# Kernel tuning notes

Measured on AMD Instinct MI355X. Metric: run time of the kernel, lower is better.

The kernel has to match this reference:

```python
import jax, jax.numpy as jnp
import numpy as np

EPS = 1e-9
THRESHOLD = 0.2          # second_policy_eval = 'threshold'
CAP_FACTOR = 2.0         # capacity_factor_eval
MIN_EXPERT_CAPACITY = 4


def setup_inputs() -> dict:
    key = jax.random.key(0)
    k1, k2 = jax.random.split(key)
    x = jax.random.normal(k1, (8, 2048, 1024), dtype=jnp.float32)
    W = jax.random.normal(k2, (1024, 64), dtype=jnp.float32) * 0.02
    return {"x": x, "W": W}


def _cumsum_exclusive(t):
    # exclusive cumsum along token dim (-2)
    return jnp.cumsum(t, axis=-2) - t


def reference(x, W):
    b, n, d = x.shape
    e = W.shape[1]
    dt = x.dtype

    raw_gates = jax.nn.softmax(jnp.einsum('bnd,de->bne', x, W), axis=-1)  # [b,n,e]

    gate_1 = jnp.max(raw_gates, axis=-1)            # [b,n]
    index_1 = jnp.argmax(raw_gates, axis=-1)        # [b,n]
    mask_1 = jax.nn.one_hot(index_1, e, dtype=dt)   # [b,n,e]
    density_1_proxy = raw_gates

    gates_wo_top1 = raw_gates * (1.0 - mask_1)
    gate_2 = jnp.max(gates_wo_top1, axis=-1)
    index_2 = jnp.argmax(gates_wo_top1, axis=-1)
    mask_2 = jax.nn.one_hot(index_2, e, dtype=dt)

    denom = gate_1 + gate_2 + EPS
    gate_1 = gate_1 / denom
    gate_2 = gate_2 / denom

    density_1 = jnp.mean(mask_1, axis=-2)                         # [b,e]
    density_1_proxy_m = jnp.mean(density_1_proxy, axis=-2)        # [b,e]
    loss = jnp.mean(density_1_proxy_m * density_1) * float(e ** 2)

    # policy == 'threshold'
    mask_2 = mask_2 * (gate_2 > THRESHOLD).astype(dt)[..., None]

    expert_capacity = max(min(n, int(n * CAP_FACTOR / e)), MIN_EXPERT_CAPACITY)
    cap_f = float(expert_capacity)

    position_in_expert_1 = _cumsum_exclusive(mask_1) * mask_1
    mask_1 = mask_1 * (position_in_expert_1 < cap_f).astype(dt)
    mask_1_count = jnp.sum(mask_1, axis=-2, keepdims=True)        # [b,1,e]
    mask_1_flat = jnp.sum(mask_1, axis=-1)                        # [b,n]
    position_in_expert_1 = jnp.sum(position_in_expert_1, axis=-1) # [b,n]
    gate_1 = gate_1 * mask_1_flat

    position_in_expert_2 = _cumsum_exclusive(mask_2) + mask_1_count
    position_in_expert_2 = position_in_expert_2 * mask_2
    mask_2 = mask_2 * (position_in_expert_2 < cap_f).astype(dt)
    mask_2_flat = jnp.sum(mask_2, axis=-1)
    position_in_expert_2 = jnp.sum(position_in_expert_2, axis=-1)
    gate_2 = gate_2 * mask_2_flat

    # combine: [b, n, e, capacity]
    oh_e1 = jax.nn.one_hot(index_1, e, dtype=dt)[..., None]                                    # [b,n,e,1]
    oh_c1 = jax.nn.one_hot(position_in_expert_1.astype(jnp.int32), expert_capacity, dtype=dt)[..., None, :]  # [b,n,1,cap]
    oh_e2 = jax.nn.one_hot(index_2, e, dtype=dt)[..., None]
    oh_c2 = jax.nn.one_hot(position_in_expert_2.astype(jnp.int32), expert_capacity, dtype=dt)[..., None, :]

    combine_tensor = (
        (gate_1 * mask_1_flat)[..., None, None] * oh_e1 * oh_c1
        + (gate_2 * mask_2_flat)[..., None, None] * oh_e2 * oh_c2
    )
    dispatch_tensor = (combine_tensor != 0).astype(dt)
    return dispatch_tensor, combine_tensor, loss
```

## Files before the change

kernel.cpp:

```cpp
#include <hip/hip_runtime.h>
#include <math.h>

#define BB 8
#define NN 2048
#define DD 1024
#define EE 64
#define CAP 64
#define NTOK (BB * NN)
#define OUT_T_FLOATS 67108864
#define OUT_T_F4     16777216


__global__ __launch_bounds__(1024, 4) void gating_kernel(
    const float* __restrict__ x, const float* __restrict__ W,
    float4* __restrict__ recs, float* __restrict__ dens)
{
    __shared__ float red[4][64][65];
    __shared__ float dred[4][64];

    const int tid  = threadIdx.x;
    const int lane = tid & 63;
    const int wave = __builtin_amdgcn_readfirstlane(tid >> 6);
    const int ks   = wave & 3;
    const int eq   = wave >> 2;
    const int tok  = blockIdx.x * 64 + lane;

    float acc[16];
#pragma unroll
    for (int j = 0; j < 16; ++j) acc[j] = 0.f;

    const float4* xq = (const float4*)(x + (size_t)tok * DD + ks * 256);
    const float*  wq = W + (size_t)(ks * 256) * EE + eq * 16;

#pragma unroll 2
    for (int c = 0; c < 64; ++c) {
        const float4 xv = xq[c];
        const float xs[4] = {xv.x, xv.y, xv.z, xv.w};
#pragma unroll
        for (int kk = 0; kk < 4; ++kk) {
            const float4* wr = (const float4*)(wq + (size_t)(c * 4 + kk) * EE);
            const float4 w0 = wr[0], w1 = wr[1], w2 = wr[2], w3 = wr[3];
            acc[ 0] = fmaf(xs[kk], w0.x, acc[ 0]);
            acc[ 1] = fmaf(xs[kk], w0.y, acc[ 1]);
            acc[ 2] = fmaf(xs[kk], w0.z, acc[ 2]);
            acc[ 3] = fmaf(xs[kk], w0.w, acc[ 3]);
            acc[ 4] = fmaf(xs[kk], w1.x, acc[ 4]);
            acc[ 5] = fmaf(xs[kk], w1.y, acc[ 5]);
            acc[ 6] = fmaf(xs[kk], w1.z, acc[ 6]);
            acc[ 7] = fmaf(xs[kk], w1.w, acc[ 7]);
            acc[ 8] = fmaf(xs[kk], w2.x, acc[ 8]);
            acc[ 9] = fmaf(xs[kk], w2.y, acc[ 9]);
            acc[10] = fmaf(xs[kk], w2.z, acc[10]);
            acc[11] = fmaf(xs[kk], w2.w, acc[11]);
            acc[12] = fmaf(xs[kk], w3.x, acc[12]);
            acc[13] = fmaf(xs[kk], w3.y, acc[13]);
            acc[14] = fmaf(xs[kk], w3.z, acc[14]);
            acc[15] = fmaf(xs[kk], w3.w, acc[15]);
        }
    }

#pragma unroll
    for (int j = 0; j < 16; ++j)
        red[ks][eq * 16 + j][lane] = acc[j];
    __syncthreads();

    if (wave < 4) {
        const int t0 = wave * 16;
        float densacc = 0.f;
#pragma unroll 1
        for (int ti = 0; ti < 16; ++ti) {
            const int t = t0 + ti;
            const float lv = ((red[0][lane][t] + red[1][lane][t])
                            + red[2][lane][t]) + red[3][lane][t];

            float v = lv; int bi = lane;
#pragma unroll
            for (int off = 32; off; off >>= 1) {
                float ov = __shfl_xor(v, off);
                int   oi = __shfl_xor(bi, off);
                if (ov > v || (ov == v && oi < bi)) { v = ov; bi = oi; }
            }
            const float m1 = v; const int i1 = bi;
            float v2 = (lane == i1) ? -INFINITY : lv; int b2 = lane;
#pragma unroll
            for (int off = 32; off; off >>= 1) {
                float ov = __shfl_xor(v2, off);
                int   oi = __shfl_xor(b2, off);
                if (ov > v2 || (ov == v2 && oi < b2)) { v2 = ov; b2 = oi; }
            }
            const float m2 = v2; const int i2 = b2;

            float ex = expf(lv - m1);
            float Z = ex;
#pragma unroll
            for (int off = 32; off; off >>= 1) Z += __shfl_xor(Z, off);
            float g1 = 1.0f / Z;
            float g2 = expf(m2 - m1) * g1;
            float den = g1 + g2 + 1e-9f;
            float g1n = g1 / den;
            float g2n = g2 / den;
            int flag = (g2n > 0.2f) ? 1 : 0;

            densacc += ex * g1;

            if (lane == 0)
                recs[blockIdx.x * 64 + t] =
                    make_float4(g1n, g2n, __int_as_float(i1),
                                __int_as_float(i2 | (flag << 8)));
        }
        dred[wave][lane] = densacc;
    }
    __syncthreads();
    if (tid < 64) {
        float s = dred[0][tid] + dred[1][tid] + dred[2][tid] + dred[3][tid];
        dens[blockIdx.x * 64 + tid] = s;
    }
}

__global__ __launch_bounds__(1024) void scan_kernel(
    const float4* __restrict__ recs, const float* __restrict__ dens,
    float4* __restrict__ frecs, float* __restrict__ lossp)
{
    const int b = blockIdx.x;
    __shared__ int hist1[32][64], pre1[32][64];
    __shared__ int hist2[32][64], pre2[32][64];
    __shared__ int base2[64];
    __shared__ float dsum[64];

    const int tid = threadIdx.x;
    const int lane = tid & 63;
    const int wave = tid >> 6;

    float4 r[2];
    int e1[2], e2[2], fl[2], rank1[2], rank2[2];
    const unsigned long long below = (1ull << lane) - 1ull;

#pragma unroll
    for (int u = 0; u < 2; ++u) {
        const int g = 2 * wave + u;
        const int tok = g * 64 + lane;
        float4 rr = recs[b * NN + tok];
        r[u] = rr;
        e1[u] = __float_as_int(rr.z);
        int i2f = __float_as_int(rr.w);
        e2[u] = i2f & 63;
        fl[u] = i2f >> 8;

        unsigned long long m = ~0ull, mv = ~0ull;
#pragma unroll
        for (int bit = 0; bit < 6; ++bit) {
            unsigned long long vt = __ballot((e1[u] >> bit) & 1);
            m  &= ((e1[u] >> bit) & 1) ? vt : ~vt;
            mv &= ((lane  >> bit) & 1) ? vt : ~vt;
        }
        rank1[u] = __popcll(m & below);
        hist1[g][lane] = __popcll(mv);

        unsigned long long fv = __ballot(fl[u]);
        m = fv; mv = fv;
#pragma unroll
        for (int bit = 0; bit < 6; ++bit) {
            unsigned long long vt = __ballot((e2[u] >> bit) & 1);
            m  &= ((e2[u] >> bit) & 1) ? vt : ~vt;
            mv &= ((lane  >> bit) & 1) ? vt : ~vt;
        }
        rank2[u] = __popcll(m & below);
        hist2[g][lane] = __popcll(mv);
    }

    if (wave == 0) {
        float s = 0.f;
        for (int k = 0; k < 32; ++k) s += dens[(b * 32 + k) * 64 + lane];
        dsum[lane] = s;
    }
    __syncthreads();

    if (wave == 0) {
        int run = 0;
#pragma unroll
        for (int g = 0; g < 32; ++g) { pre1[g][lane] = run; run += hist1[g][lane]; }
        base2[lane] = run < CAP ? run : CAP;
        int run2 = 0;
#pragma unroll
        for (int g = 0; g < 32; ++g) { pre2[g][lane] = run2; run2 += hist2[g][lane]; }
        float v = dsum[lane] * (float)run;
#pragma unroll
        for (int off = 32; off; off >>= 1) v += __shfl_xor(v, off);
        if (lane == 0) lossp[b] = v;
    }
    __syncthreads();

#pragma unroll
    for (int u = 0; u < 2; ++u) {
        const int g = 2 * wave + u;
        const int tok = g * 64 + lane;
        int p1 = rank1[u] + pre1[g][e1[u]];
        int k1 = p1 < CAP;
        int p2 = rank2[u] + pre2[g][e2[u]] + base2[e2[u]];
        int k2 = fl[u] && (p2 < CAP);
        float4 fr;
        fr.x = k1 ? r[u].x : 0.f;
        fr.y = k2 ? r[u].y : 0.f;
        fr.z = __int_as_float(k1 ? (e1[u] * CAP + p1) : -1);
        fr.w = __int_as_float(k2 ? (e2[u] * CAP + p2) : -1);
        frecs[b * NN + tok] = fr;
    }
}

__global__ __launch_bounds__(256) void fill_kernel(
    const float4* __restrict__ frecs, const float* __restrict__ lossp,
    float* __restrict__ out)
{
    const int tid = blockIdx.x * 256 + threadIdx.x;
    const int token = tid >> 10;
    const int e  = (tid >> 4) & 63;
    const int c4 = tid & 15;
    float4 r = frecs[token];

    float cx = 0.f, cy = 0.f, cz = 0.f, cw = 0.f;
    float dx = 0.f, dy = 0.f, dz = 0.f, dw = 0.f;

    int p1 = __float_as_int(r.z);
    if (p1 >= 0 && (p1 >> 6) == e && ((p1 >> 2) & 15) == c4) {
        int cc = p1 & 3;
        if      (cc == 0) { cx = r.x; dx = 1.f; }
        else if (cc == 1) { cy = r.x; dy = 1.f; }
        else if (cc == 2) { cz = r.x; dz = 1.f; }
        else              { cw = r.x; dw = 1.f; }
    }
    int p2 = __float_as_int(r.w);
    if (p2 >= 0 && (p2 >> 6) == e && ((p2 >> 2) & 15) == c4) {
        int cc = p2 & 3;
        if      (cc == 0) { cx = r.y; dx = 1.f; }
        else if (cc == 1) { cy = r.y; dy = 1.f; }
        else if (cc == 2) { cz = r.y; dz = 1.f; }
        else              { cw = r.y; dw = 1.f; }
    }

    float4* o4 = (float4*)out;
    o4[tid]             = make_float4(dx, dy, dz, dw);
    o4[tid + OUT_T_F4]  = make_float4(cx, cy, cz, cw);

    if (tid == 0) {
        float s = 0.f;
        for (int k = 0; k < 8; ++k) s += lossp[k];
        out[2 * (size_t)OUT_T_FLOATS] = s * (1.0f / 524288.0f);
    }
}

extern "C" void kernel_launch(void* const* d_in, const int* in_sizes, int n_in,
                              void* d_out, int out_size, void* d_ws, size_t ws_size,
                              hipStream_t stream)
{
    const float* x = (const float*)d_in[0];
    const float* W = (const float*)d_in[1];
    float* out = (float*)d_out;
    char* ws = (char*)d_ws;

    float4* recs  = (float4*)(ws);
    float4* frecs = (float4*)(ws + 262144);
    float*  dens  = (float*)(ws + 524288);
    float*  lossp = (float*)(ws + 589824);

    gating_kernel<<<256, 1024, 0, stream>>>(x, W, recs, dens);
    scan_kernel<<<8, 1024, 0, stream>>>(recs, dens, frecs, lossp);
    fill_kernel<<<65536, 256, 0, stream>>>(frecs, lossp, out);
}
```

Measured before the change: 609.2 us.

## Stage x tiles in swizzled shared memory and use grid-stride nontemporal fill

```diff
diff --git a/kernel.cpp b/kernel.cpp
--- a/kernel.cpp
+++ b/kernel.cpp
@@ -10,11 +10,14 @@
 #define OUT_T_FLOATS 67108864
 #define OUT_T_F4     16777216
 
+typedef float f32x4 __attribute__((ext_vector_type(4)));
+
 
 __global__ __launch_bounds__(1024, 4) void gating_kernel(
     const float* __restrict__ x, const float* __restrict__ W,
     float4* __restrict__ recs, float* __restrict__ dens)
 {
+    __shared__ float lxs[2][64][128];
     __shared__ float red[4][64][65];
     __shared__ float dred[4][64];
 
@@ -23,40 +26,72 @@
     const int wave = __builtin_amdgcn_readfirstlane(tid >> 6);
     const int ks   = wave & 3;
     const int eq   = wave >> 2;
-    const int tok  = blockIdx.x * 64 + lane;
+    const int tok0 = blockIdx.x * 64;
+
+    const int p  = tid & 31;
+    const int r0 = tid >> 5;
+    const int r1 = r0 + 32;
+    const int g0 = p ^ (r0 & 7);
+    const float* src0 = x + (size_t)(tok0 + r0) * DD + (size_t)g0 * 4;
+    const float* src1 = x + (size_t)(tok0 + r1) * DD + (size_t)g0 * 4;
 
     float acc[16];
 #pragma unroll
     for (int j = 0; j < 16; ++j) acc[j] = 0.f;
 
-    const float4* xq = (const float4*)(x + (size_t)tok * DD + ks * 256);
-    const float*  wq = W + (size_t)(ks * 256) * EE + eq * 16;
-
-#pragma unroll 2
-    for (int c = 0; c < 64; ++c) {
-        const float4 xv = xq[c];
-        const float xs[4] = {xv.x, xv.y, xv.z, xv.w};
-#pragma unroll
-        for (int kk = 0; kk < 4; ++kk) {
-            const float4* wr = (const float4*)(wq + (size_t)(c * 4 + kk) * EE);
-            const float4 w0 = wr[0], w1 = wr[1], w2 = wr[2], w3 = wr[3];
-            acc[ 0] = fmaf(xs[kk], w0.x, acc[ 0]);
-            acc[ 1] = fmaf(xs[kk], w0.y, acc[ 1]);
-            acc[ 2] = fmaf(xs[kk], w0.z, acc[ 2]);
-            acc[ 3] = fmaf(xs[kk], w0.w, acc[ 3]);
-            acc[ 4] = fmaf(xs[kk], w1.x, acc[ 4]);
-            acc[ 5] = fmaf(xs[kk], w1.y, acc[ 5]);
-            acc[ 6] = fmaf(xs[kk], w1.z, acc[ 6]);
-            acc[ 7] = fmaf(xs[kk], w1.w, acc[ 7]);
-            acc[ 8] = fmaf(xs[kk], w2.x, acc[ 8]);
-            acc[ 9] = fmaf(xs[kk], w2.y, acc[ 9]);
-            acc[10] = fmaf(xs[kk], w2.z, acc[10]);
-            acc[11] = fmaf(xs[kk], w2.w, acc[11]);
-            acc[12] = fmaf(xs[kk], w3.x, acc[12]);
-            acc[13] = fmaf(xs[kk], w3.y, acc[13]);
-            acc[14] = fmaf(xs[kk], w3.z, acc[14]);
-            acc[15] = fmaf(xs[kk], w3.w, acc[15]);
-        }
+    {
+        const float4 v0 = *(const float4*)src0;
+        const float4 v1 = *(const float4*)src1;
+        *((float4*)&lxs[0][r0][0] + p) = v0;
+        *((float4*)&lxs[0][r1][0] + p) = v1;
+    }
+    __syncthreads();
+
+    int cur = 0;
+#pragma unroll 1
+    for (int step = 0; step < 8; ++step) {
+        float4 n0, n1;
+        if (step < 7) {
+            n0 = *(const float4*)(src0 + (size_t)(step + 1) * 128);
+            n1 = *(const float4*)(src1 + (size_t)(step + 1) * 128);
+        }
+
+        const float* wbase = W + (size_t)(step * 128 + ks * 32) * EE + eq * 16;
+#pragma unroll
+        for (int kqi = 0; kqi < 8; ++kqi) {
+            const int kq = ks * 8 + kqi;
+            const float4 xv = *((const float4*)&lxs[cur][lane][0] + (kq ^ (lane & 7)));
+            const float xs[4] = {xv.x, xv.y, xv.z, xv.w};
+            const float* wr = wbase + (size_t)(kqi * 4) * EE;
+#pragma unroll
+            for (int kk = 0; kk < 4; ++kk) {
+                const float4* w4 = (const float4*)(wr + (size_t)kk * EE);
+                const float4 w0 = w4[0], w1 = w4[1], w2 = w4[2], w3 = w4[3];
+                acc[ 0] = fmaf(xs[kk], w0.x, acc[ 0]);
+                acc[ 1] = fmaf(xs[kk], w0.y, acc[ 1]);
+                acc[ 2] = fmaf(xs[kk], w0.z, acc[ 2]);
+                acc[ 3] = fmaf(xs[kk], w0.w, acc[ 3]);
+                acc[ 4] = fmaf(xs[kk], w1.x, acc[ 4]);
+                acc[ 5] = fmaf(xs[kk], w1.y, acc[ 5]);
+                acc[ 6] = fmaf(xs[kk], w1.z, acc[ 6]);
+                acc[ 7] = fmaf(xs[kk], w1.w, acc[ 7]);
+                acc[ 8] = fmaf(xs[kk], w2.x, acc[ 8]);
+                acc[ 9] = fmaf(xs[kk], w2.y, acc[ 9]);
+                acc[10] = fmaf(xs[kk], w2.z, acc[10]);
+                acc[11] = fmaf(xs[kk], w2.w, acc[11]);
+                acc[12] = fmaf(xs[kk], w3.x, acc[12]);
+                acc[13] = fmaf(xs[kk], w3.y, acc[13]);
+                acc[14] = fmaf(xs[kk], w3.z, acc[14]);
+                acc[15] = fmaf(xs[kk], w3.w, acc[15]);
+            }
+        }
+
+        if (step < 7) {
+            *((float4*)&lxs[cur ^ 1][r0][0] + p) = n0;
+            *((float4*)&lxs[cur ^ 1][r1][0] + p) = n1;
+        }
+        __syncthreads();
+        cur ^= 1;
     }
 
 #pragma unroll
@@ -211,37 +246,41 @@
     const float4* __restrict__ frecs, const float* __restrict__ lossp,
     float* __restrict__ out)
 {
-    const int tid = blockIdx.x * 256 + threadIdx.x;
-    const int token = tid >> 10;
-    const int e  = (tid >> 4) & 63;
-    const int c4 = tid & 15;
-    float4 r = frecs[token];
-
-    float cx = 0.f, cy = 0.f, cz = 0.f, cw = 0.f;
-    float dx = 0.f, dy = 0.f, dz = 0.f, dw = 0.f;
-
-    int p1 = __float_as_int(r.z);
-    if (p1 >= 0 && (p1 >> 6) == e && ((p1 >> 2) & 15) == c4) {
-        int cc = p1 & 3;
-        if      (cc == 0) { cx = r.x; dx = 1.f; }
-        else if (cc == 1) { cy = r.x; dy = 1.f; }
-        else if (cc == 2) { cz = r.x; dz = 1.f; }
-        else              { cw = r.x; dw = 1.f; }
-    }
-    int p2 = __float_as_int(r.w);
-    if (p2 >= 0 && (p2 >> 6) == e && ((p2 >> 2) & 15) == c4) {
-        int cc = p2 & 3;
-        if      (cc == 0) { cx = r.y; dx = 1.f; }
-        else if (cc == 1) { cy = r.y; dy = 1.f; }
-        else if (cc == 2) { cz = r.y; dz = 1.f; }
-        else              { cw = r.y; dw = 1.f; }
-    }
-
-    float4* o4 = (float4*)out;
-    o4[tid]             = make_float4(dx, dy, dz, dw);
-    o4[tid + OUT_T_F4]  = make_float4(cx, cy, cz, cw);
-
-    if (tid == 0) {
+    f32x4* o4 = (f32x4*)out;
+    const int stride = gridDim.x * 256;
+
+    for (int tid = blockIdx.x * 256 + threadIdx.x; tid < OUT_T_F4; tid += stride) {
+        const int e  = (tid >> 4) & 63;
+        const int c4 = tid & 15;
+        float4 r = frecs[tid >> 10];
+
+        float cx = 0.f, cy = 0.f, cz = 0.f, cw = 0.f;
+        float dx = 0.f, dy = 0.f, dz = 0.f, dw = 0.f;
+
+        int p1 = __float_as_int(r.z);
+        if (p1 >= 0 && (p1 >> 6) == e && ((p1 >> 2) & 15) == c4) {
+            int cc = p1 & 3;
+            if      (cc == 0) { cx = r.x; dx = 1.f; }
+            else if (cc == 1) { cy = r.x; dy = 1.f; }
+            else if (cc == 2) { cz = r.x; dz = 1.f; }
+            else              { cw = r.x; dw = 1.f; }
+        }
+        int p2 = __float_as_int(r.w);
+        if (p2 >= 0 && (p2 >> 6) == e && ((p2 >> 2) & 15) == c4) {
+            int cc = p2 & 3;
+            if      (cc == 0) { cx = r.y; dx = 1.f; }
+            else if (cc == 1) { cy = r.y; dy = 1.f; }
+            else if (cc == 2) { cz = r.y; dz = 1.f; }
+            else              { cw = r.y; dw = 1.f; }
+        }
+
+        f32x4 dv = {dx, dy, dz, dw};
+        f32x4 cv = {cx, cy, cz, cw};
+        __builtin_nontemporal_store(dv, &o4[tid]);
+        __builtin_nontemporal_store(cv, &o4[tid + OUT_T_F4]);
+    }
+
+    if (blockIdx.x == 0 && threadIdx.x == 0) {
         float s = 0.f;
         for (int k = 0; k < 8; ++k) s += lossp[k];
         out[2 * (size_t)OUT_T_FLOATS] = s * (1.0f / 524288.0f);
@@ -264,5 +303,5 @@
 
     gating_kernel<<<256, 1024, 0, stream>>>(x, W, recs, dens);
     scan_kernel<<<8, 1024, 0, stream>>>(recs, dens, frecs, lossp);
-    fill_kernel<<<65536, 256, 0, stream>>>(frecs, lossp, out);
+    fill_kernel<<<2048, 256, 0, stream>>>(frecs, lossp, out);
 }
```

New measurement: 703.6 us. 1.15x slower.
